# Performance work log

Measured on AMD Instinct MI355X. Metric: run time of the kernel, lower is better.

Reference implementation:

```python
import jax, jax.numpy as jnp
import numpy as np

D = 512    # feature_dim
NH = 8     # n_head
LQ = 1024  # query length
LK = 1024  # key/value length
B = 4      # batch
TEMP = 30.0


def setup_inputs() -> dict:
    key = jax.random.key(0)
    ks = jax.random.split(key, 10)
    s = (2.0 / D) ** 0.5  # init: normal(0, sqrt(2/out_features))
    t = lambda k, shp: jax.random.normal(k, shp, dtype=jnp.float32)
    return {
        'query_real': t(ks[0], (LQ, B, D)),
        'query_imag': t(ks[1], (LQ, B, D)),
        'key_real': t(ks[2], (LK, B, D)),
        'key_imag': t(ks[3], (LK, B, D)),
        'value_real': t(ks[4], (LK, B, D)),
        'value_imag': t(ks[5], (LK, B, D)),
        # per-head stacked Linear weights [NH, out, in] (torch Linear: x @ W.T + b)
        'WK_real': t(ks[6], (NH, D, D)) * s,
        'WK_imag': t(ks[7], (NH, D, D)) * s,
        'WV_real': t(ks[8], (NH, D, D)) * s,
        'WV_imag': t(ks[9], (NH, D, D)) * s,
        'bK_real': jnp.zeros((NH, D), jnp.float32),
        'bK_imag': jnp.zeros((NH, D), jnp.float32),
        'bV_real': jnp.zeros((NH, D), jnp.float32),
        'bV_imag': jnp.zeros((NH, D), jnp.float32),
    }


def reference(query_real, query_imag, key_real, key_imag, value_real, value_imag,
              WK_real, WK_imag, WV_real, WV_imag,
              bK_real, bK_imag, bV_real, bV_imag):
    # stacked per-head linear: x [L,B,D], W [H,E,D], b [H,E] -> [H,L,B,E]
    lin = lambda x, W, b: jnp.einsum('lbd,hed->hlbe', x, W) + b[:, None, None, :]
    # complex projection of keys with WK (real/imag parts)
    kr = lin(key_real, WK_real, bK_real) - lin(key_imag, WK_imag, bK_imag)
    ki = lin(key_real, WK_imag, bK_imag) + lin(key_imag, WK_real, bK_real)
    # queries are projected with the WV weights (as in the source)
    qr = lin(query_real, WV_real, bV_real) - lin(query_imag, WV_imag, bV_imag)
    qi = lin(query_real, WV_imag, bV_imag) + lin(query_imag, WV_real, bV_real)
    # complex dot product q*k (no conjugate), magnitude -> scores [H,B,Lq,Lk]
    dr = jnp.einsum('hqbd,hpbd->hbqp', qr, kr) - jnp.einsum('hqbd,hpbd->hbqp', qi, ki)
    di = jnp.einsum('hqbd,hpbd->hbqp', qi, kr) + jnp.einsum('hqbd,hpbd->hbqp', qr, ki)
    mag = jnp.sqrt(dr * dr + di * di)
    aff = jax.nn.softmax(mag * TEMP, axis=-1)  # softmax over keys
    # weighted value sum; values are the RAW inputs (not projected)
    out_real = jnp.einsum('hbqp,pbd->qbhd', aff, value_real).reshape(LQ, B, NH * D)
    out_imag = jnp.einsum('hbqp,pbd->qbhd', aff, value_imag).reshape(LQ, B, NH * D)
    return out_real, out_imag
```

## Files before the change

kernel.cpp:

```cpp
#include <hip/hip_runtime.h>
#include <math.h>

typedef _Float16 h8_t __attribute__((ext_vector_type(8)));
typedef _Float16 h4_t __attribute__((ext_vector_type(4)));
typedef float    f4_t __attribute__((ext_vector_type(4)));

#define MFMA16(a, b, c) __builtin_amdgcn_mfma_f32_16x16x32_f16((a), (b), (c), 0, 0, 0)

typedef const __attribute__((address_space(1))) void* gas1_t;
typedef __attribute__((address_space(3))) void* las3_t;
__device__ __forceinline__ void gload16(const void* g, void* l) {
  __builtin_amdgcn_global_load_lds((gas1_t)g, (las3_t)l, 16, 0, 0);
}

constexpr int L   = 1024;
constexpr int NB  = 4;
constexpr int NHh = 8;
constexpr int D   = 512;
constexpr int M1  = L * NB;
constexpr int K1  = 2 * D;
constexpr int N1  = NHh * 2 * D;
constexpr int HB  = NHh * NB;

constexpr size_t PL_A2 = (size_t)HB * L * K1 * 2;
constexpr size_t PL_BS = (size_t)HB * 3 * L * D * 2;
constexpr size_t OFF_R0 = 0;
constexpr size_t OFF_A2 = 134217728;
constexpr size_t OFF_BS = OFF_A2 + 2 * PL_A2;
constexpr size_t OFF_VT = OFF_BS + 2 * PL_BS;
constexpr size_t WS_NEED = OFF_VT + (size_t)NB * 1024 * 1024 * 2;
constexpr size_t PL_AX = (size_t)M1 * K1 * 2;
constexpr size_t ST_AQ = 0;
constexpr size_t ST_AK = 2 * PL_AX;
constexpr size_t PL_W  = (size_t)N1 * K1 * 2;
constexpr size_t ST_WQ = 4 * PL_AX;
constexpr size_t ST_WK = ST_WQ + 2 * PL_W;

static __device__ __forceinline__ void split32(float x, _Float16& hi, _Float16& lo) {
  _Float16 h = (_Float16)x;
  hi = h;
  lo = (_Float16)(x - (float)h);
}


__global__ void k_stage_x(const float* __restrict__ qre, const float* __restrict__ qim,
                          const float* __restrict__ kre, const float* __restrict__ kim,
                          _Float16* __restrict__ qhi, _Float16* __restrict__ qlo,
                          _Float16* __restrict__ khi, _Float16* __restrict__ klo) {
  const float* re; const float* im; _Float16* hi; _Float16* lo;
  if (blockIdx.y == 0) { re = qre; im = qim; hi = qhi; lo = qlo; }
  else                 { re = kre; im = kim; hi = khi; lo = klo; }
  int t = blockIdx.x * 256 + threadIdx.x;
  size_t idx = (size_t)t * 4;
  int m = (int)(idx >> 10), k = (int)(idx & 1023);
  const float* src = (k < 512) ? (re + (size_t)m * 512 + k) : (im + (size_t)m * 512 + (k - 512));
  f4_t v = *reinterpret_cast<const f4_t*>(src);
  h4_t h, l;
#pragma unroll
  for (int j = 0; j < 4; ++j) {
    _Float16 hh, ll; split32(v[j], hh, ll); h[j] = hh; l[j] = ll;
  }
  int sw = ((m >> 1) & 3) << 3;
  size_t dst = (size_t)m * 1024 + (k ^ sw);
  *reinterpret_cast<h4_t*>(hi + dst) = h;
  *reinterpret_cast<h4_t*>(lo + dst) = l;
}

__global__ void k_stage_w(const float* __restrict__ WVr, const float* __restrict__ WVi,
                          const float* __restrict__ WKr, const float* __restrict__ WKi,
                          _Float16* __restrict__ qhi, _Float16* __restrict__ qlo,
                          _Float16* __restrict__ khi, _Float16* __restrict__ klo) {
  const float* Wr; const float* Wi; _Float16* hi; _Float16* lo;
  if (blockIdx.y == 0) { Wr = WVr; Wi = WVi; hi = qhi; lo = qlo; }
  else                 { Wr = WKr; Wi = WKi; hi = khi; lo = klo; }
  int t = blockIdx.x * 256 + threadIdx.x;
  size_t idx = (size_t)t * 4;
  int n = (int)(idx >> 10), k = (int)(idx & 1023);
  int h = n >> 10, ri = (n >> 9) & 1, e = n & 511;
  size_t rowoff = ((size_t)(h * 512 + e)) * 512;
  const float* src; float sgn = 1.0f;
  if (ri == 0) {
    if (k < 512) src = Wr + rowoff + k;
    else { src = Wi + rowoff + (k - 512); sgn = -1.0f; }
  } else {
    if (k < 512) src = Wi + rowoff + k;
    else src = Wr + rowoff + (k - 512);
  }
  f4_t v = *reinterpret_cast<const f4_t*>(src);
  h4_t h4, l4;
#pragma unroll
  for (int j = 0; j < 4; ++j) {
    _Float16 hh, ll; split32(sgn * v[j], hh, ll); h4[j] = hh; l4[j] = ll;
  }
  int sw = ((n >> 1) & 3) << 3;
  size_t dst = (size_t)n * 1024 + (k ^ sw);
  *reinterpret_cast<h4_t*>(hi + dst) = h4;
  *reinterpret_cast<h4_t*>(lo + dst) = l4;
}

__global__ void k_stage_v(const float* __restrict__ vr, const float* __restrict__ vi,
                          _Float16* __restrict__ vt) {
  __shared__ float tile[64][65];
  int pt = blockIdx.x, nt = blockIdx.y, b = blockIdx.z;
  const float* src = (nt < 8) ? vr : vi;
  int dbase = (nt & 7) * 64;
  for (int i = threadIdx.x; i < 4096; i += 256) {
    int pl = i >> 6, dl = i & 63;
    tile[pl][dl] = src[((size_t)(pt * 64 + pl) * 4 + b) * 512 + dbase + dl];
  }
  __syncthreads();
  for (int i = threadIdx.x; i < 4096; i += 256) {
    int nl = i >> 6, pl = i & 63;
    int psw = pl ^ ((nl & 7) << 3);
    vt[((size_t)b * 1024 + nt * 64 + nl) * 1024 + pt * 64 + psw] = (_Float16)tile[pl][nl];
  }
}

__global__ __launch_bounds__(512, 1) void k_proj(
    const _Float16* __restrict__ Ahi, const _Float16* __restrict__ Alo,
    const _Float16* __restrict__ Bhi, const _Float16* __restrict__ Blo,
    const float* __restrict__ biasR, const float* __restrict__ biasI,
    _Float16* __restrict__ OutHi, _Float16* __restrict__ OutLo, int mode) {
  extern __shared__ __align__(16) _Float16 dldsP[];
  const int tid = threadIdx.x;
  const int id = blockIdx.x;
  const int xcd = id & 7, j = id >> 3;
  const int cm = j >> 2, cn = j & 3;
  const int m0 = cm * 256;
  const int n0 = (xcd * 4 + cn) * 256;
  const int wid = tid >> 6, lane = tid & 63;
  const int wm = (wid >> 1) * 64, wn = (wid & 1) * 128;
  const int fr = lane & 15, fq = lane >> 4;
  const int csw = (fq ^ ((fr >> 1) & 3)) * 8;

  const int srow = tid >> 2, sslot = tid & 3;
  const int soff = srow * 32 + sslot * 8;
  const _Float16* gA0 = Ahi + (size_t)(m0 + srow) * 1024 + sslot * 8;
  const _Float16* gA1 = gA0 + 128 * 1024;
  const _Float16* gA2 = Alo + (size_t)(m0 + srow) * 1024 + sslot * 8;
  const _Float16* gA3 = gA2 + 128 * 1024;
  const _Float16* gB0 = Bhi + (size_t)(n0 + srow) * 1024 + sslot * 8;
  const _Float16* gB1 = gB0 + 128 * 1024;
  const _Float16* gB2 = Blo + (size_t)(n0 + srow) * 1024 + sslot * 8;
  const _Float16* gB3 = gB2 + 128 * 1024;

  auto STAGE_A = [&](int buf) {
    _Float16* Lb = dldsP + buf * 32768;
    gload16(gA0, &Lb[soff]);
    gload16(gA1, &Lb[4096 + soff]);
    gload16(gA2, &Lb[8192 + soff]);
    gload16(gA3, &Lb[12288 + soff]);
    gA0 += 32; gA1 += 32; gA2 += 32; gA3 += 32;
  };
  auto STAGE_B = [&](int buf) {
    _Float16* Lb = dldsP + buf * 32768;
    gload16(gB0, &Lb[16384 + soff]);
    gload16(gB1, &Lb[20480 + soff]);
    gload16(gB2, &Lb[24576 + soff]);
    gload16(gB3, &Lb[28672 + soff]);
    gB0 += 32; gB1 += 32; gB2 += 32; gB3 += 32;
  };

  f4_t acc[4][8] = {};

  STAGE_A(0); STAGE_B(0);
  asm volatile("s_waitcnt vmcnt(0)" ::: "memory");
  __builtin_amdgcn_s_barrier();

  for (int kt = 0; kt < 32; ++kt) {
    const int cur = kt & 1, nxt = cur ^ 1;
    const _Float16* Lb = dldsP + cur * 32768;
    h8_t af[4][2];
#pragma unroll
    for (int mi = 0; mi < 4; ++mi) {
      int r = wm + mi * 16 + fr;
      af[mi][0] = *reinterpret_cast<const h8_t*>(&Lb[r * 32 + csw]);
      af[mi][1] = *reinterpret_cast<const h8_t*>(&Lb[8192 + r * 32 + csw]);
    }
    h8_t bh[4], bl[4];
#pragma unroll
    for (int ni = 0; ni < 4; ++ni) {
      int rn = wn + ni * 16 + fr;
      bh[ni] = *reinterpret_cast<const h8_t*>(&Lb[16384 + rn * 32 + csw]);
      bl[ni] = *reinterpret_cast<const h8_t*>(&Lb[24576 + rn * 32 + csw]);
    }
    if (kt < 31) STAGE_A(nxt);
    __builtin_amdgcn_s_barrier();
    __builtin_amdgcn_s_setprio(1);
#pragma unroll
    for (int ni = 0; ni < 4; ++ni)
#pragma unroll
      for (int mi = 0; mi < 4; ++mi) {
        acc[mi][ni] = MFMA16(af[mi][0], bh[ni], acc[mi][ni]);
        acc[mi][ni] = MFMA16(af[mi][0], bl[ni], acc[mi][ni]);
        acc[mi][ni] = MFMA16(af[mi][1], bh[ni], acc[mi][ni]);
      }
    __builtin_amdgcn_s_setprio(0);
    __builtin_amdgcn_s_barrier();
#pragma unroll
    for (int ni = 0; ni < 4; ++ni) {
      int rn = wn + (ni + 4) * 16 + fr;
      bh[ni] = *reinterpret_cast<const h8_t*>(&Lb[16384 + rn * 32 + csw]);
      bl[ni] = *reinterpret_cast<const h8_t*>(&Lb[24576 + rn * 32 + csw]);
    }
    if (kt < 31) STAGE_B(nxt);
    __builtin_amdgcn_s_barrier();
    __builtin_amdgcn_s_setprio(1);
#pragma unroll
    for (int ni = 0; ni < 4; ++ni)
#pragma unroll
      for (int mi = 0; mi < 4; ++mi) {
        acc[mi][ni + 4] = MFMA16(af[mi][0], bh[ni], acc[mi][ni + 4]);
        acc[mi][ni + 4] = MFMA16(af[mi][0], bl[ni], acc[mi][ni + 4]);
        acc[mi][ni + 4] = MFMA16(af[mi][1], bh[ni], acc[mi][ni + 4]);
      }
    __builtin_amdgcn_s_setprio(0);
    if (kt < 31) asm volatile("s_waitcnt vmcnt(0)" ::: "memory");
    __builtin_amdgcn_s_barrier();
  }

#pragma unroll
  for (int mi = 0; mi < 4; ++mi)
#pragma unroll
    for (int ni = 0; ni < 8; ++ni)
#pragma unroll
      for (int r = 0; r < 4; ++r) {
        int m = m0 + wm + mi * 16 + fq * 4 + r;
        int n = n0 + wn + ni * 16 + fr;
        int h = n >> 10, ri = (n >> 9) & 1, e = n & 511;
        float bias = (ri == 0) ? (biasR[h * 512 + e] - biasI[h * 512 + e])
                               : (biasI[h * 512 + e] + biasR[h * 512 + e]);
        float val = acc[mi][ni][r] + bias;
        _Float16 hi, lo; split32(val, hi, lo);
        int lb = m & 3;
        int lrow = m >> 2;
        int hb = h * 4 + lb;
        int sw = ((lrow >> 1) & 3) << 3;
        if (mode == 0) {
          size_t dst = ((size_t)hb * 1024 + lrow) * 1024 + ((ri * 512 + e) ^ sw);
          OutHi[dst] = hi; OutLo[dst] = lo;
        } else {
          int esw = e ^ sw;
          if (ri == 0) {
            size_t dst = (((size_t)hb * 3 + 0) * 1024 + lrow) * 512 + esw;
            OutHi[dst] = hi; OutLo[dst] = lo;
          } else {
            size_t d1 = (((size_t)hb * 3 + 1) * 1024 + lrow) * 512 + esw;
            size_t d2 = (((size_t)hb * 3 + 2) * 1024 + lrow) * 512 + esw;
            OutHi[d1] = hi;  OutLo[d1] = lo;
            OutHi[d2] = -hi; OutLo[d2] = -lo;
          }
        }
      }
}

__global__ __launch_bounds__(512, 1) void k_score(
    const _Float16* __restrict__ A2hi, const _Float16* __restrict__ A2lo,
    const _Float16* __restrict__ BShi, const _Float16* __restrict__ BSlo,
    float* __restrict__ mag) {
  extern __shared__ __align__(16) _Float16 dldsS[];
  const int tid = threadIdx.x;
  const int id = blockIdx.x;
  const int xcd = id & 7, j = id >> 3;
  const int hb = xcd * 4 + (j >> 5);
  const int r5 = j & 31;
  const int m0 = (r5 >> 3) * 256, n0 = (r5 & 7) * 128;
  const int wid = tid >> 6, lane = tid & 63;
  const int wm = (wid >> 1) * 64, wn = (wid & 1) * 64;
  const int fr = lane & 15, fq = lane >> 4;
  const int csw = (fq ^ ((fr >> 1) & 3)) * 8;

  const _Float16* Abh = A2hi + (size_t)hb * 1048576;
  const _Float16* Abl = A2lo + (size_t)hb * 1048576;
  const _Float16* BShb = BShi + (size_t)hb * 3 * 524288;
  const _Float16* BSlb = BSlo + (size_t)hb * 3 * 524288;

  const int srow = tid >> 2, sslot = tid & 3;
  const int soff = srow * 32 + sslot * 8;
  const size_t bbase = (size_t)(n0 + srow) * 512 + sslot * 8;
  const _Float16* gA0 = Abh + (size_t)(m0 + srow) * 1024 + sslot * 8;
  const _Float16* gA1 = gA0 + 128 * 1024;
  const _Float16* gA2 = Abl + (size_t)(m0 + srow) * 1024 + sslot * 8;
  const _Float16* gA3 = gA2 + 128 * 1024;
  const _Float16* gB0 = BShb + bbase;
  const _Float16* gB1 = BSlb + bbase;
  const _Float16* gB2 = BShb + 524288 + bbase;
  const _Float16* gB3 = BSlb + 524288 + bbase;

  auto STAGE_A = [&](int buf) {
    _Float16* Lb = dldsS + buf * 32768;
    gload16(gA0, &Lb[soff]);
    gload16(gA1, &Lb[4096 + soff]);
    gload16(gA2, &Lb[8192 + soff]);
    gload16(gA3, &Lb[12288 + soff]);
    gA0 += 32; gA1 += 32; gA2 += 32; gA3 += 32;
  };
  auto STAGE_B = [&](int buf, int kt) {
    if (kt == 16) {
      gB0 = BShb + 2 * 524288 + bbase;
      gB1 = BSlb + 2 * 524288 + bbase;
      gB2 = BShb + bbase;
      gB3 = BSlb + bbase;
    }
    _Float16* Lb = dldsS + buf * 32768;
    gload16(gB0, &Lb[16384 + soff]);
    gload16(gB1, &Lb[20480 + soff]);
    gload16(gB2, &Lb[24576 + soff]);
    gload16(gB3, &Lb[28672 + soff]);
    gB0 += 32; gB1 += 32; gB2 += 32; gB3 += 32;
  };

  f4_t adr[4][4] = {}, adi[4][4] = {};

  STAGE_A(0); STAGE_B(0, 0);
  asm volatile("s_waitcnt vmcnt(0)" ::: "memory");
  __builtin_amdgcn_s_barrier();

  for (int kt = 0; kt < 32; ++kt) {
    const int cur = kt & 1, nxt = cur ^ 1;
    const _Float16* Lb = dldsS + cur * 32768;
    h8_t af[4][2];
#pragma unroll
    for (int mi = 0; mi < 4; ++mi) {
      int r = wm + mi * 16 + fr;
      af[mi][0] = *reinterpret_cast<const h8_t*>(&Lb[r * 32 + csw]);
      af[mi][1] = *reinterpret_cast<const h8_t*>(&Lb[8192 + r * 32 + csw]);
    }
    h8_t drh[2], drl[2], dih[2], dil[2];
#pragma unroll
    for (int ni = 0; ni < 2; ++ni) {
      int rn = wn + ni * 16 + fr;
      drh[ni] = *reinterpret_cast<const h8_t*>(&Lb[16384 + rn * 32 + csw]);
      drl[ni] = *reinterpret_cast<const h8_t*>(&Lb[20480 + rn * 32 + csw]);
      dih[ni] = *reinterpret_cast<const h8_t*>(&Lb[24576 + rn * 32 + csw]);
      dil[ni] = *reinterpret_cast<const h8_t*>(&Lb[28672 + rn * 32 + csw]);
    }
    if (kt < 31) STAGE_A(nxt);
    __builtin_amdgcn_s_barrier();
    __builtin_amdgcn_s_setprio(1);
#pragma unroll
    for (int ni = 0; ni < 2; ++ni)
#pragma unroll
      for (int mi = 0; mi < 4; ++mi) {
        adr[mi][ni] = MFMA16(af[mi][0], drh[ni], adr[mi][ni]);
        adr[mi][ni] = MFMA16(af[mi][0], drl[ni], adr[mi][ni]);
        adr[mi][ni] = MFMA16(af[mi][1], drh[ni], adr[mi][ni]);
        adi[mi][ni] = MFMA16(af[mi][0], dih[ni], adi[mi][ni]);
        adi[mi][ni] = MFMA16(af[mi][0], dil[ni], adi[mi][ni]);
        adi[mi][ni] = MFMA16(af[mi][1], dih[ni], adi[mi][ni]);
      }
    __builtin_amdgcn_s_setprio(0);
    __builtin_amdgcn_s_barrier();
#pragma unroll
    for (int ni = 0; ni < 2; ++ni) {
      int rn = wn + (ni + 2) * 16 + fr;
      drh[ni] = *reinterpret_cast<const h8_t*>(&Lb[16384 + rn * 32 + csw]);
      drl[ni] = *reinterpret_cast<const h8_t*>(&Lb[20480 + rn * 32 + csw]);
      dih[ni] = *reinterpret_cast<const h8_t*>(&Lb[24576 + rn * 32 + csw]);
      dil[ni] = *reinterpret_cast<const h8_t*>(&Lb[28672 + rn * 32 + csw]);
    }
    if (kt < 31) STAGE_B(nxt, kt + 1);
    __builtin_amdgcn_s_barrier();
    __builtin_amdgcn_s_setprio(1);
#pragma unroll
    for (int ni = 0; ni < 2; ++ni)
#pragma unroll
      for (int mi = 0; mi < 4; ++mi) {
        adr[mi][ni + 2] = MFMA16(af[mi][0], drh[ni], adr[mi][ni + 2]);
        adr[mi][ni + 2] = MFMA16(af[mi][0], drl[ni], adr[mi][ni + 2]);
        adr[mi][ni + 2] = MFMA16(af[mi][1], drh[ni], adr[mi][ni + 2]);
        adi[mi][ni + 2] = MFMA16(af[mi][0], dih[ni], adi[mi][ni + 2]);
        adi[mi][ni + 2] = MFMA16(af[mi][0], dil[ni], adi[mi][ni + 2]);
        adi[mi][ni + 2] = MFMA16(af[mi][1], dih[ni], adi[mi][ni + 2]);
      }
    __builtin_amdgcn_s_setprio(0);
    if (kt < 31) asm volatile("s_waitcnt vmcnt(0)" ::: "memory");
    __builtin_amdgcn_s_barrier();
  }

  float* mb = mag + (size_t)hb * 1048576;
#pragma unroll
  for (int mi = 0; mi < 4; ++mi)
#pragma unroll
    for (int ni = 0; ni < 4; ++ni)
#pragma unroll
      for (int r = 0; r < 4; ++r) {
        int q = m0 + wm + mi * 16 + fq * 4 + r;
        int p = n0 + wn + ni * 16 + fr;
        float dr = adr[mi][ni][r], di = adi[mi][ni][r];
        mb[(size_t)q * 1024 + p] = sqrtf(dr * dr + di * di) * 30.0f;
      }
}

__global__ void k_softmax(const float* __restrict__ mag, _Float16* __restrict__ aff) {
  const size_t base = (size_t)blockIdx.x * 1024;
  const int q = blockIdx.x & 1023;
  const int sw = (q & 7) << 3;
  const int tid = threadIdx.x;
  const int wid = tid >> 6, lane = tid & 63;
  float v[4];
#pragma unroll
  for (int j = 0; j < 4; ++j) v[j] = mag[base + tid + j * 256];
  float mx = fmaxf(fmaxf(v[0], v[1]), fmaxf(v[2], v[3]));
#pragma unroll
  for (int o = 32; o > 0; o >>= 1) mx = fmaxf(mx, __shfl_xor(mx, o));
  __shared__ float red[8];
  if (lane == 0) red[wid] = mx;
  __syncthreads();
  mx = fmaxf(fmaxf(red[0], red[1]), fmaxf(red[2], red[3]));
  float e[4]; float s = 0.0f;
#pragma unroll
  for (int j = 0; j < 4; ++j) { e[j] = __expf(v[j] - mx); s += e[j]; }
#pragma unroll
  for (int o = 32; o > 0; o >>= 1) s += __shfl_xor(s, o);
  if (lane == 0) red[4 + wid] = s;
  __syncthreads();
  s = red[4] + red[5] + red[6] + red[7];
  float inv = 1.0f / s;
#pragma unroll
  for (int j = 0; j < 4; ++j) aff[base + j * 256 + (tid ^ sw)] = (_Float16)(e[j] * inv);
}

__global__ __launch_bounds__(256, 2) void k_pv(
    const _Float16* __restrict__ aff, const _Float16* __restrict__ vt,
    float* __restrict__ out) {
  extern __shared__ __align__(16) _Float16 dldsV[];
  const int tid = threadIdx.x;
  const int id = blockIdx.x;
  const int xcd = id & 7, j = id >> 3;
  const int b = xcd >> 1;
  const int h = (xcd & 1) * 4 + (j >> 6);
  const int hb = h * 4 + b;
  const int r6 = j & 63;
  const int m0 = (r6 >> 3) * 128, n0 = (r6 & 7) * 128;
  const int wid = tid >> 6, lane = tid & 63;
  const int wm = (wid >> 1) * 64, wn = (wid & 1) * 64;
  const int fr = lane & 15, fq = lane >> 4;
  const int s7 = fr & 7;

  const _Float16* Ab = aff + (size_t)hb * 1048576;
  const _Float16* Bb = vt + (size_t)b * 1048576;

  const int srow = tid >> 3, sslot = tid & 7;
  const int soff = srow * 64 + sslot * 8;
  const _Float16* gA = Ab + (size_t)(m0 + srow) * 1024 + sslot * 8;
  const _Float16* gB = Bb + (size_t)(n0 + srow) * 1024 + sslot * 8;

  auto STAGE = [&](int buf) {
    _Float16* Lb = dldsV + buf * 16384;
    gload16(gA,             &Lb[soff]);
    gload16(gA + 32 * 1024, &Lb[2048 + soff]);
    gload16(gA + 64 * 1024, &Lb[4096 + soff]);
    gload16(gA + 96 * 1024, &Lb[6144 + soff]);
    gload16(gB,             &Lb[8192 + soff]);
    gload16(gB + 32 * 1024, &Lb[10240 + soff]);
    gload16(gB + 64 * 1024, &Lb[12288 + soff]);
    gload16(gB + 96 * 1024, &Lb[14336 + soff]);
    gA += 64; gB += 64;
  };

  f4_t acc[4][4] = {};
  auto compute = [&](int buf) {
    const _Float16* Lb = dldsV + buf * 16384;
#pragma unroll
    for (int k32 = 0; k32 < 2; ++k32) {
      const int csw = ((k32 * 4 + fq) ^ s7) * 8;
      h8_t af[4];
#pragma unroll
      for (int mi = 0; mi < 4; ++mi)
        af[mi] = *reinterpret_cast<const h8_t*>(&Lb[(wm + mi * 16 + fr) * 64 + csw]);
#pragma unroll
      for (int ni = 0; ni < 4; ++ni) {
        h8_t bf = *reinterpret_cast<const h8_t*>(&Lb[8192 + (wn + ni * 16 + fr) * 64 + csw]);
#pragma unroll
        for (int mi = 0; mi < 4; ++mi) acc[mi][ni] = MFMA16(af[mi], bf, acc[mi][ni]);
      }
    }
  };

  STAGE(0);
  for (int kt = 0; kt < 15; ++kt) {
    __builtin_amdgcn_s_barrier();
    STAGE((kt + 1) & 1);
    asm volatile("s_waitcnt vmcnt(8)" ::: "memory");
    __builtin_amdgcn_s_barrier();
    compute(kt & 1);
  }
  __builtin_amdgcn_s_barrier();
  asm volatile("s_waitcnt vmcnt(0)" ::: "memory");
  __builtin_amdgcn_s_barrier();
  compute(1);

#pragma unroll
  for (int mi = 0; mi < 4; ++mi)
#pragma unroll
    for (int ni = 0; ni < 4; ++ni)
#pragma unroll
      for (int r = 0; r < 4; ++r) {
        int q = m0 + wm + mi * 16 + fq * 4 + r;
        int n = n0 + wn + ni * 16 + fr;
        int d = n & 511;
        size_t o = (size_t)(n < 512 ? 0 : 16777216) + (((size_t)q * 4 + b) * 8 + h) * 512 + d;
        out[o] = acc[mi][ni][r];
      }
}

extern "C" void kernel_launch(void* const* d_in, const int* in_sizes, int n_in,
                              void* d_out, int out_size, void* d_ws, size_t ws_size,
                              hipStream_t stream) {
  (void)in_sizes; (void)n_in; (void)out_size;
  if (ws_size < WS_NEED) return;

  hipFuncSetAttribute((const void*)k_score, hipFuncAttributeMaxDynamicSharedMemorySize, 131072);
  hipFuncSetAttribute((const void*)k_proj,  hipFuncAttributeMaxDynamicSharedMemorySize, 131072);
  hipFuncSetAttribute((const void*)k_pv,    hipFuncAttributeMaxDynamicSharedMemorySize, 65536);

  const float* qre = (const float*)d_in[0];
  const float* qim = (const float*)d_in[1];
  const float* kre = (const float*)d_in[2];
  const float* kim = (const float*)d_in[3];
  const float* vre = (const float*)d_in[4];
  const float* vim = (const float*)d_in[5];
  const float* WKr = (const float*)d_in[6];
  const float* WKi = (const float*)d_in[7];
  const float* WVr = (const float*)d_in[8];
  const float* WVi = (const float*)d_in[9];
  const float* bKr = (const float*)d_in[10];
  const float* bKi = (const float*)d_in[11];
  const float* bVr = (const float*)d_in[12];
  const float* bVi = (const float*)d_in[13];

  char* ws = (char*)d_ws;
  _Float16* AqHi = (_Float16*)(ws + ST_AQ);
  _Float16* AqLo = (_Float16*)(ws + ST_AQ + PL_AX);
  _Float16* AkHi = (_Float16*)(ws + ST_AK);
  _Float16* AkLo = (_Float16*)(ws + ST_AK + PL_AX);
  _Float16* WqHi = (_Float16*)(ws + ST_WQ);
  _Float16* WqLo = (_Float16*)(ws + ST_WQ + PL_W);
  _Float16* WkHi = (_Float16*)(ws + ST_WK);
  _Float16* WkLo = (_Float16*)(ws + ST_WK + PL_W);
  _Float16* A2Hi = (_Float16*)(ws + OFF_A2);
  _Float16* A2Lo = (_Float16*)(ws + OFF_A2 + PL_A2);
  _Float16* BSHi = (_Float16*)(ws + OFF_BS);
  _Float16* BSLo = (_Float16*)(ws + OFF_BS + PL_BS);
  _Float16* Vt   = (_Float16*)(ws + OFF_VT);
  float*    magp = (float*)(ws + OFF_R0);
  _Float16* affp = (_Float16*)(ws + OFF_A2);
  float*    outp = (float*)d_out;

  k_stage_x<<<dim3(4096, 2), dim3(256), 0, stream>>>(qre, qim, kre, kim, AqHi, AqLo, AkHi, AkLo);
  k_stage_w<<<dim3(8192, 2), dim3(256), 0, stream>>>(WVr, WVi, WKr, WKi, WqHi, WqLo, WkHi, WkLo);
  k_stage_v<<<dim3(16, 16, 4), dim3(256), 0, stream>>>(vre, vim, Vt);
  k_proj<<<dim3(512), dim3(512), 131072, stream>>>(AqHi, AqLo, WqHi, WqLo, bVr, bVi, A2Hi, A2Lo, 0);
  k_proj<<<dim3(512), dim3(512), 131072, stream>>>(AkHi, AkLo, WkHi, WkLo, bKr, bKi, BSHi, BSLo, 1);
  k_score<<<dim3(1024), dim3(512), 131072, stream>>>(A2Hi, A2Lo, BSHi, BSLo, magp);
  k_softmax<<<dim3(32 * 1024), dim3(256), 0, stream>>>(magp, affp);
  k_pv<<<dim3(2048), dim3(256), 65536, stream>>>(affp, Vt, outp);
}
```

Measured before the change: 907.8 us.

## Pre-pack projection outputs into MFMA fragment layout and use 32x32 MFMA in score

The projection kernels now write Q and K operands directly in a fragment-packed layout that matches the 32x32x16 MFMA lane ordering, with hi and lo interleaved per tile. The score kernel switches from 16x16x32 to 32x32x16 MFMA, stages contiguous blocks with straight global-to-LDS copies, and reads fragments with simple lane-linear LDS loads instead of swizzled row reads. The aim is fewer LDS reads per MFMA and simpler address arithmetic, at the cost of scattered writes in the projection epilogue and a new barrier per K half-step.

```diff
diff --git a/kernel.cpp b/kernel.cpp
--- a/kernel.cpp
+++ b/kernel.cpp
@@ -4,8 +4,10 @@
 typedef _Float16 h8_t __attribute__((ext_vector_type(8)));
 typedef _Float16 h4_t __attribute__((ext_vector_type(4)));
 typedef float    f4_t __attribute__((ext_vector_type(4)));
+typedef float    fx16 __attribute__((ext_vector_type(16)));
 
 #define MFMA16(a, b, c) __builtin_amdgcn_mfma_f32_16x16x32_f16((a), (b), (c), 0, 0, 0)
+#define MFMA32(a, b, c) __builtin_amdgcn_mfma_f32_32x32x16_f16((a), (b), (c), 0, 0, 0)
 
 typedef const __attribute__((address_space(1))) void* gas1_t;
 typedef __attribute__((address_space(3))) void* las3_t;
@@ -35,6 +37,13 @@
 constexpr size_t PL_W  = (size_t)N1 * K1 * 2;
 constexpr size_t ST_WQ = 4 * PL_AX;
 constexpr size_t ST_WK = ST_WQ + 2 * PL_W;
+
+constexpr size_t A2_HB = 2097152;
+constexpr size_t A2_MT = 524288;
+constexpr size_t A2_KT = 16384;
+constexpr size_t BS_PANE = 1048576;
+constexpr size_t BS_NT = 131072;
+constexpr size_t BS_KQ = 8192;
 
 static __device__ __forceinline__ void split32(float x, _Float16& hi, _Float16& lo) {
   _Float16 h = (_Float16)x;
@@ -120,7 +129,7 @@
     const _Float16* __restrict__ Ahi, const _Float16* __restrict__ Alo,
     const _Float16* __restrict__ Bhi, const _Float16* __restrict__ Blo,
     const float* __restrict__ biasR, const float* __restrict__ biasI,
-    _Float16* __restrict__ OutHi, _Float16* __restrict__ OutLo, int mode) {
+    _Float16* __restrict__ Out, int mode) {
   extern __shared__ __align__(16) _Float16 dldsP[];
   const int tid = threadIdx.x;
   const int id = blockIdx.x;
@@ -233,30 +242,42 @@
         float val = acc[mi][ni][r] + bias;
         _Float16 hi, lo; split32(val, hi, lo);
         int lb = m & 3;
-        int lrow = m >> 2;
+        int qrow = m >> 2;
         int hb = h * 4 + lb;
-        int sw = ((lrow >> 1) & 3) << 3;
         if (mode == 0) {
-          size_t dst = ((size_t)hb * 1024 + lrow) * 1024 + ((ri * 512 + e) ^ sw);
-          OutHi[dst] = hi; OutLo[dst] = lo;
+          int c = ri * 512 + e;
+          int mt = qrow >> 8, mb = (qrow >> 5) & 7;
+          int kt = c >> 5, kh = (c >> 4) & 1;
+          int lane2 = (((c >> 3) & 1) << 5) | (qrow & 31);
+          int elem = c & 7;
+          size_t base = (size_t)hb * A2_HB + (size_t)mt * A2_MT + (size_t)kt * A2_KT;
+          size_t ofh = base + (size_t)(((0 * 8 + mb) * 2 + kh) * 512 + lane2 * 8 + elem);
+          size_t ofl = base + (size_t)(((1 * 8 + mb) * 2 + kh) * 512 + lane2 * 8 + elem);
+          Out[ofh] = hi; Out[ofl] = lo;
         } else {
-          int esw = e ^ sw;
+          int prow = qrow;
+          int nt = prow >> 7, nb = (prow >> 5) & 3;
+          int kq = e >> 5, kh = (e >> 4) & 1;
+          int lane2 = (((e >> 3) & 1) << 5) | (prow & 31);
+          int elem = e & 7;
+          size_t inner_h = (size_t)(((0 * 4 + nb) * 2 + kh) * 512 + lane2 * 8 + elem);
+          size_t inner_l = (size_t)(((1 * 4 + nb) * 2 + kh) * 512 + lane2 * 8 + elem);
+          size_t blk = (size_t)nt * BS_NT + (size_t)kq * BS_KQ;
           if (ri == 0) {
-            size_t dst = (((size_t)hb * 3 + 0) * 1024 + lrow) * 512 + esw;
-            OutHi[dst] = hi; OutLo[dst] = lo;
+            size_t pb = (size_t)(hb * 3 + 0) * BS_PANE + blk;
+            Out[pb + inner_h] = hi; Out[pb + inner_l] = lo;
           } else {
-            size_t d1 = (((size_t)hb * 3 + 1) * 1024 + lrow) * 512 + esw;
-            size_t d2 = (((size_t)hb * 3 + 2) * 1024 + lrow) * 512 + esw;
-            OutHi[d1] = hi;  OutLo[d1] = lo;
-            OutHi[d2] = -hi; OutLo[d2] = -lo;
+            size_t p1 = (size_t)(hb * 3 + 1) * BS_PANE + blk;
+            size_t p2 = (size_t)(hb * 3 + 2) * BS_PANE + blk;
+            Out[p1 + inner_h] = hi;  Out[p1 + inner_l] = lo;
+            Out[p2 + inner_h] = -hi; Out[p2 + inner_l] = -lo;
           }
         }
       }
 }
 
 __global__ __launch_bounds__(512, 1) void k_score(
-    const _Float16* __restrict__ A2hi, const _Float16* __restrict__ A2lo,
-    const _Float16* __restrict__ BShi, const _Float16* __restrict__ BSlo,
+    const _Float16* __restrict__ A2g, const _Float16* __restrict__ BSg,
     float* __restrict__ mag) {
   extern __shared__ __align__(16) _Float16 dldsS[];
   const int tid = threadIdx.x;
@@ -264,130 +285,97 @@
   const int xcd = id & 7, j = id >> 3;
   const int hb = xcd * 4 + (j >> 5);
   const int r5 = j & 31;
-  const int m0 = (r5 >> 3) * 256, n0 = (r5 & 7) * 128;
+  const int mt = r5 >> 3, nt = r5 & 7;
+  const int m0 = mt * 256, n0 = nt * 128;
   const int wid = tid >> 6, lane = tid & 63;
-  const int wm = (wid >> 1) * 64, wn = (wid & 1) * 64;
-  const int fr = lane & 15, fq = lane >> 4;
-  const int csw = (fq ^ ((fr >> 1) & 3)) * 8;
-
-  const _Float16* Abh = A2hi + (size_t)hb * 1048576;
-  const _Float16* Abl = A2lo + (size_t)hb * 1048576;
-  const _Float16* BShb = BShi + (size_t)hb * 3 * 524288;
-  const _Float16* BSlb = BSlo + (size_t)hb * 3 * 524288;
-
-  const int srow = tid >> 2, sslot = tid & 3;
-  const int soff = srow * 32 + sslot * 8;
-  const size_t bbase = (size_t)(n0 + srow) * 512 + sslot * 8;
-  const _Float16* gA0 = Abh + (size_t)(m0 + srow) * 1024 + sslot * 8;
-  const _Float16* gA1 = gA0 + 128 * 1024;
-  const _Float16* gA2 = Abl + (size_t)(m0 + srow) * 1024 + sslot * 8;
-  const _Float16* gA3 = gA2 + 128 * 1024;
-  const _Float16* gB0 = BShb + bbase;
-  const _Float16* gB1 = BSlb + bbase;
-  const _Float16* gB2 = BShb + 524288 + bbase;
-  const _Float16* gB3 = BSlb + 524288 + bbase;
-
-  auto STAGE_A = [&](int buf) {
-    _Float16* Lb = dldsS + buf * 32768;
-    gload16(gA0, &Lb[soff]);
-    gload16(gA1, &Lb[4096 + soff]);
-    gload16(gA2, &Lb[8192 + soff]);
-    gload16(gA3, &Lb[12288 + soff]);
-    gA0 += 32; gA1 += 32; gA2 += 32; gA3 += 32;
+  const int mg = wid >> 1;
+  const int ng = wid & 1;
+
+  const _Float16* Abase = A2g + (size_t)hb * A2_HB + (size_t)mt * A2_MT;
+  const _Float16* Bp0 = BSg + (size_t)(hb * 3 + 0) * BS_PANE + (size_t)nt * BS_NT;
+  const _Float16* Bp1 = BSg + (size_t)(hb * 3 + 1) * BS_PANE + (size_t)nt * BS_NT;
+  const _Float16* Bp2 = BSg + (size_t)(hb * 3 + 2) * BS_PANE + (size_t)nt * BS_NT;
+
+  auto STAGE_A = [&](int buf, int ktn) {
+    const _Float16* s = Abase + (size_t)ktn * A2_KT + tid * 8;
+    _Float16* d = dldsS + buf * 32768 + tid * 8;
+    gload16(s,          d);
+    gload16(s + 4096,   d + 4096);
+    gload16(s + 8192,   d + 8192);
+    gload16(s + 12288,  d + 12288);
   };
-  auto STAGE_B = [&](int buf, int kt) {
-    if (kt == 16) {
-      gB0 = BShb + 2 * 524288 + bbase;
-      gB1 = BSlb + 2 * 524288 + bbase;
-      gB2 = BShb + bbase;
-      gB3 = BSlb + bbase;
-    }
-    _Float16* Lb = dldsS + buf * 32768;
-    gload16(gB0, &Lb[16384 + soff]);
-    gload16(gB1, &Lb[20480 + soff]);
-    gload16(gB2, &Lb[24576 + soff]);
-    gload16(gB3, &Lb[28672 + soff]);
-    gB0 += 32; gB1 += 32; gB2 += 32; gB3 += 32;
+  auto STAGE_B = [&](int buf, int ktn) {
+    const int kq = ktn & 15;
+    const _Float16* pdr = (ktn < 16 ? Bp0 : Bp2) + (size_t)kq * BS_KQ + tid * 8;
+    const _Float16* pdi = (ktn < 16 ? Bp1 : Bp0) + (size_t)kq * BS_KQ + tid * 8;
+    _Float16* d = dldsS + buf * 32768 + tid * 8;
+    gload16(pdr,        d + 16384);
+    gload16(pdr + 4096, d + 20480);
+    gload16(pdi,        d + 24576);
+    gload16(pdi + 4096, d + 28672);
   };
 
-  f4_t adr[4][4] = {}, adi[4][4] = {};
-
-  STAGE_A(0); STAGE_B(0, 0);
+  fx16 adr[2][2] = {}, adi[2][2] = {};
+
+  STAGE_A(0, 0); STAGE_B(0, 0);
   asm volatile("s_waitcnt vmcnt(0)" ::: "memory");
   __builtin_amdgcn_s_barrier();
 
   for (int kt = 0; kt < 32; ++kt) {
     const int cur = kt & 1, nxt = cur ^ 1;
-    const _Float16* Lb = dldsS + cur * 32768;
-    h8_t af[4][2];
-#pragma unroll
-    for (int mi = 0; mi < 4; ++mi) {
-      int r = wm + mi * 16 + fr;
-      af[mi][0] = *reinterpret_cast<const h8_t*>(&Lb[r * 32 + csw]);
-      af[mi][1] = *reinterpret_cast<const h8_t*>(&Lb[8192 + r * 32 + csw]);
+    const _Float16* Lc = dldsS + cur * 32768;
+#pragma unroll
+    for (int kh = 0; kh < 2; ++kh) {
+      h8_t a[2][2], bd[2][2], bi[2][2];
+#pragma unroll
+      for (int mi = 0; mi < 2; ++mi)
+#pragma unroll
+        for (int p = 0; p < 2; ++p)
+          a[mi][p] = *reinterpret_cast<const h8_t*>(
+              &Lc[((p * 8 + mg * 2 + mi) * 2 + kh) * 512 + lane * 8]);
+#pragma unroll
+      for (int ni = 0; ni < 2; ++ni)
+#pragma unroll
+        for (int p = 0; p < 2; ++p) {
+          bd[ni][p] = *reinterpret_cast<const h8_t*>(
+              &Lc[16384 + ((p * 4 + ng * 2 + ni) * 2 + kh) * 512 + lane * 8]);
+          bi[ni][p] = *reinterpret_cast<const h8_t*>(
+              &Lc[24576 + ((p * 4 + ng * 2 + ni) * 2 + kh) * 512 + lane * 8]);
+        }
+      if (kh == 0) { if (kt < 31) STAGE_A(nxt, kt + 1); }
+      else         { if (kt < 31) STAGE_B(nxt, kt + 1); }
+      __builtin_amdgcn_s_barrier();
+      __builtin_amdgcn_s_setprio(1);
+#pragma unroll
+      for (int ni = 0; ni < 2; ++ni)
+#pragma unroll
+        for (int mi = 0; mi < 2; ++mi) {
+          adr[mi][ni] = MFMA32(a[mi][0], bd[ni][0], adr[mi][ni]);
+          adr[mi][ni] = MFMA32(a[mi][0], bd[ni][1], adr[mi][ni]);
+          adr[mi][ni] = MFMA32(a[mi][1], bd[ni][0], adr[mi][ni]);
+          adi[mi][ni] = MFMA32(a[mi][0], bi[ni][0], adi[mi][ni]);
+          adi[mi][ni] = MFMA32(a[mi][0], bi[ni][1], adi[mi][ni]);
+          adi[mi][ni] = MFMA32(a[mi][1], bi[ni][0], adi[mi][ni]);
+        }
+      __builtin_amdgcn_s_setprio(0);
+      if (kh == 1 && kt < 31) asm volatile("s_waitcnt vmcnt(0)" ::: "memory");
+      __builtin_amdgcn_s_barrier();
     }
-    h8_t drh[2], drl[2], dih[2], dil[2];
-#pragma unroll
-    for (int ni = 0; ni < 2; ++ni) {
-      int rn = wn + ni * 16 + fr;
-      drh[ni] = *reinterpret_cast<const h8_t*>(&Lb[16384 + rn * 32 + csw]);
-      drl[ni] = *reinterpret_cast<const h8_t*>(&Lb[20480 + rn * 32 + csw]);
-      dih[ni] = *reinterpret_cast<const h8_t*>(&Lb[24576 + rn * 32 + csw]);
-      dil[ni] = *reinterpret_cast<const h8_t*>(&Lb[28672 + rn * 32 + csw]);
-    }
-    if (kt < 31) STAGE_A(nxt);
-    __builtin_amdgcn_s_barrier();
-    __builtin_amdgcn_s_setprio(1);
+  }
+
+  float* mb = mag + (size_t)hb * 1048576;
+  const int col = lane & 31;
+  const int rbase = 4 * (lane >> 5);
+#pragma unroll
+  for (int mi = 0; mi < 2; ++mi)
 #pragma unroll
     for (int ni = 0; ni < 2; ++ni)
 #pragma unroll
-      for (int mi = 0; mi < 4; ++mi) {
-        adr[mi][ni] = MFMA16(af[mi][0], drh[ni], adr[mi][ni]);
-        adr[mi][ni] = MFMA16(af[mi][0], drl[ni], adr[mi][ni]);
-        adr[mi][ni] = MFMA16(af[mi][1], drh[ni], adr[mi][ni]);
-        adi[mi][ni] = MFMA16(af[mi][0], dih[ni], adi[mi][ni]);
-        adi[mi][ni] = MFMA16(af[mi][0], dil[ni], adi[mi][ni]);
-        adi[mi][ni] = MFMA16(af[mi][1], dih[ni], adi[mi][ni]);
-      }
-    __builtin_amdgcn_s_setprio(0);
-    __builtin_amdgcn_s_barrier();
-#pragma unroll
-    for (int ni = 0; ni < 2; ++ni) {
-      int rn = wn + (ni + 2) * 16 + fr;
-      drh[ni] = *reinterpret_cast<const h8_t*>(&Lb[16384 + rn * 32 + csw]);
-      drl[ni] = *reinterpret_cast<const h8_t*>(&Lb[20480 + rn * 32 + csw]);
-      dih[ni] = *reinterpret_cast<const h8_t*>(&Lb[24576 + rn * 32 + csw]);
-      dil[ni] = *reinterpret_cast<const h8_t*>(&Lb[28672 + rn * 32 + csw]);
-    }
-    if (kt < 31) STAGE_B(nxt, kt + 1);
-    __builtin_amdgcn_s_barrier();
-    __builtin_amdgcn_s_setprio(1);
-#pragma unroll
-    for (int ni = 0; ni < 2; ++ni)
-#pragma unroll
-      for (int mi = 0; mi < 4; ++mi) {
-        adr[mi][ni + 2] = MFMA16(af[mi][0], drh[ni], adr[mi][ni + 2]);
-        adr[mi][ni + 2] = MFMA16(af[mi][0], drl[ni], adr[mi][ni + 2]);
-        adr[mi][ni + 2] = MFMA16(af[mi][1], drh[ni], adr[mi][ni + 2]);
-        adi[mi][ni + 2] = MFMA16(af[mi][0], dih[ni], adi[mi][ni + 2]);
-        adi[mi][ni + 2] = MFMA16(af[mi][0], dil[ni], adi[mi][ni + 2]);
-        adi[mi][ni + 2] = MFMA16(af[mi][1], dih[ni], adi[mi][ni + 2]);
-      }
-    __builtin_amdgcn_s_setprio(0);
-    if (kt < 31) asm volatile("s_waitcnt vmcnt(0)" ::: "memory");
-    __builtin_amdgcn_s_barrier();
-  }
-
-  float* mb = mag + (size_t)hb * 1048576;
-#pragma unroll
-  for (int mi = 0; mi < 4; ++mi)
-#pragma unroll
-    for (int ni = 0; ni < 4; ++ni)
-#pragma unroll
-      for (int r = 0; r < 4; ++r) {
-        int q = m0 + wm + mi * 16 + fq * 4 + r;
-        int p = n0 + wn + ni * 16 + fr;
-        float dr = adr[mi][ni][r], di = adi[mi][ni][r];
+      for (int reg = 0; reg < 16; ++reg) {
+        int row = (reg & 3) + 8 * (reg >> 2) + rbase;
+        int q = m0 + mg * 64 + mi * 32 + row;
+        int p = n0 + ng * 64 + ni * 32 + col;
+        float dr = adr[mi][ni][reg], di = adi[mi][ni][reg];
         mb[(size_t)q * 1024 + p] = sqrtf(dr * dr + di * di) * 30.0f;
       }
 }
@@ -539,10 +527,8 @@
   _Float16* WqLo = (_Float16*)(ws + ST_WQ + PL_W);
   _Float16* WkHi = (_Float16*)(ws + ST_WK);
   _Float16* WkLo = (_Float16*)(ws + ST_WK + PL_W);
-  _Float16* A2Hi = (_Float16*)(ws + OFF_A2);
-  _Float16* A2Lo = (_Float16*)(ws + OFF_A2 + PL_A2);
-  _Float16* BSHi = (_Float16*)(ws + OFF_BS);
-  _Float16* BSLo = (_Float16*)(ws + OFF_BS + PL_BS);
+  _Float16* A2g  = (_Float16*)(ws + OFF_A2);
+  _Float16* BSg  = (_Float16*)(ws + OFF_BS);
   _Float16* Vt   = (_Float16*)(ws + OFF_VT);
   float*    magp = (float*)(ws + OFF_R0);
   _Float16* affp = (_Float16*)(ws + OFF_A2);
@@ -551,9 +537,9 @@
   k_stage_x<<<dim3(4096, 2), dim3(256), 0, stream>>>(qre, qim, kre, kim, AqHi, AqLo, AkHi, AkLo);
   k_stage_w<<<dim3(8192, 2), dim3(256), 0, stream>>>(WVr, WVi, WKr, WKi, WqHi, WqLo, WkHi, WkLo);
   k_stage_v<<<dim3(16, 16, 4), dim3(256), 0, stream>>>(vre, vim, Vt);
-  k_proj<<<dim3(512), dim3(512), 131072, stream>>>(AqHi, AqLo, WqHi, WqLo, bVr, bVi, A2Hi, A2Lo, 0);
-  k_proj<<<dim3(512), dim3(512), 131072, stream>>>(AkHi, AkLo, WkHi, WkLo, bKr, bKi, BSHi, BSLo, 1);
-  k_score<<<dim3(1024), dim3(512), 131072, stream>>>(A2Hi, A2Lo, BSHi, BSLo, magp);
+  k_proj<<<dim3(512), dim3(512), 131072, stream>>>(AqHi, AqLo, WqHi, WqLo, bVr, bVi, A2g, 0);
+  k_proj<<<dim3(512), dim3(512), 131072, stream>>>(AkHi, AkLo, WkHi, WkLo, bKr, bKi, BSg, 1);
+  k_score<<<dim3(1024), dim3(512), 131072, stream>>>(A2g, BSg, magp);
   k_softmax<<<dim3(32 * 1024), dim3(256), 0, stream>>>(magp, affp);
   k_pv<<<dim3(2048), dim3(256), 65536, stream>>>(affp, Vt, outp);
 }
```

Result: no change. 922.3 us (+1.6%).
